# Optimization experiments

Hardware: AMD Instinct MI355X
Metric: run time of the kernel (lower is better)

## Reference

```python
import math
import jax, jax.numpy as jnp
import numpy as np

B, P, L, R = 16, 256, 8, 128  # n_embd = L*R = 1024
H = 4 * L * R                 # MLP hidden = 4096

def new_gelu(x):
    # tanh-approx GELU as in NewGELU
    c = math.sqrt(2.0 / math.pi)
    return 0.5 * x * (1.0 + jnp.tanh(c * (x + 0.044715 * x * x * x)))

def setup_inputs() -> dict:
    key = jax.random.key(0)
    k1, k2, k3 = jax.random.split(key, 3)
    x = jax.random.normal(k1, (B, P, L, R), dtype=jnp.float32)
    W1 = jax.random.normal(k2, (L * R, H), dtype=jnp.float32) * 0.02
    b1 = jnp.zeros((H,), dtype=jnp.float32)
    W2 = jax.random.normal(k3, (H, R), dtype=jnp.float32) * 0.02
    b2 = jnp.zeros((R,), dtype=jnp.float32)
    return {"x": x, "W1": W1, "b1": b1, "W2": W2, "b2": b2}

def reference(x, W1, b1, W2, b2):
    b, p, l, r = x.shape
    flat = x.reshape(b, p, l * r)                       # [B,P,L*R]
    # Level i input = flat with first i*R entries zeroed (zeros-pad + tail slice)
    col = jnp.arange(l * r)
    mask = (col[None, :] >= (jnp.arange(l) * r)[:, None]).astype(x.dtype)  # [L, L*R]
    inp = flat[:, :, None, :] * mask                    # [B,P,L,L*R]
    h = new_gelu(jnp.einsum('bple,eh->bplh', inp, W1) + b1)  # [B,P,L,H]
    out = jnp.einsum('bplh,hr->bplr', h, W2) + b2       # [B,P,L,R]
    return out
```

## Files before the change

### kernel.cpp

```cpp
#include <hip/hip_runtime.h>
#include <hip/hip_bf16.h>


typedef _Float16 half8 __attribute__((ext_vector_type(8)));
typedef _Float16 half4 __attribute__((ext_vector_type(4)));
typedef _Float16 half2v __attribute__((ext_vector_type(2)));
typedef float    f32x4  __attribute__((ext_vector_type(4)));
typedef float    f32x16 __attribute__((ext_vector_type(16)));

#define MFMA3216(A,B,C) __builtin_amdgcn_mfma_f32_32x32x16_f16(A, B, C, 0, 0, 0)
#define MFMA1632(A,B,C) __builtin_amdgcn_mfma_f32_16x16x32_f16(A, B, C, 0, 0, 0)

__device__ __forceinline__ float gelu_f(float x){
  float t2 = x * fmaf(x*x, -0.10294324f, -2.30220842f);
  float e  = __builtin_amdgcn_exp2f(t2);
  return x * __builtin_amdgcn_rcpf(1.0f + e);
}

#define XROW 1028

__global__ void k_prep(const float* __restrict__ x, const float* __restrict__ w1,
                       const float* __restrict__ w2,
                       _Float16* __restrict__ xt, _Float16* __restrict__ w1t,
                       _Float16* __restrict__ w2t){
  __shared__ _Float16 Xs[32*XROW];
  int bid = blockIdx.x;
  int t   = threadIdx.x;
  if (bid < 128){
    const float4* x4 = reinterpret_cast<const float4*>(x) + (size_t)bid*8192;
    #pragma unroll
    for (int i = 0; i < 32; ++i){
      float4 v = x4[i*256 + t];
      half4 h;
      h[0]=(_Float16)v.x; h[1]=(_Float16)v.y; h[2]=(_Float16)v.z; h[3]=(_Float16)v.w;
      *reinterpret_cast<half4*>(Xs + i*XROW + t*4) = h;
    }
    __syncthreads();
    #pragma unroll
    for (int f = 0; f < 16; ++f){
      int fragidx = f*256 + t;
      int lane = fragidx & 63, kf = fragidx >> 6;
      int tok32 = lane & 31;
      int k = kf*16 + (lane >> 5)*8;
      half8 v = *reinterpret_cast<const half8*>(Xs + tok32*XROW + k);
      *reinterpret_cast<half8*>(xt + ((size_t)bid*4096 + fragidx)*8) = v;
    }
  } else if (bid < 2176){
    int tid = (bid - 128)*256 + t;
    int lane = tid & 63;
    int ht   = (tid >> 6) & 15;
    int kf   = (tid >> 10) & 63;
    int hq   = tid >> 16;
    int n = hq*512 + ht*32 + (lane & 31);
    int k = kf*16 + (lane >> 5)*8;
    half8 v;
    #pragma unroll
    for (int jj = 0; jj < 8; ++jj) v[jj] = (_Float16)w1[(size_t)(k + jj)*4096 + n];
    *reinterpret_cast<half8*>(w1t + (size_t)tid*8) = v;
  } else {
    int tid = (bid - 2176)*256 + t;
    int lane = tid & 63;
    int tile = tid >> 6;
    int ntr = tile & 7, kt2 = tile >> 3;
    int n = ntr*16 + (lane & 15);
    int k = kt2*32 + (lane >> 4)*8;
    half8 v;
    #pragma unroll
    for (int jj = 0; jj < 8; ++jj) v[jj] = (_Float16)w2[(size_t)(k + jj)*128 + n];
    *reinterpret_cast<half8*>(w2t + (size_t)tid*8) = v;
  }
}

__global__ void k_init_out(const float* __restrict__ b2, float* __restrict__ out){
  int i = blockIdx.x*256 + threadIdx.x;
  float4 bv = reinterpret_cast<const float4*>(b2)[i & 31];
  reinterpret_cast<float4*>(out)[i] = bv;
}

__global__ void k_reduce(const unsigned* __restrict__ part, const float* __restrict__ b2,
                         float* __restrict__ out){
  int tid = blockIdx.x*256 + threadIdx.x;
  int m16 = tid & 15;
  int rw  = (tid >> 4) & 7;
  int q   = (tid >> 7) & 3;
  int tp  = (tid >> 9) & 1;
  int i   = (tid >> 10) & 3;
  int j   = (tid >> 12) & 7;
  int tt  = tid >> 15;
  float s0 = 0.f, s1 = 0.f;
  #pragma unroll
  for (int hq = 0; hq < 8; ++hq){
    unsigned v = __builtin_nontemporal_load(part + (size_t)hq*2097152 + tid);
    half2v h = __builtin_bit_cast(half2v, v);
    s0 += (float)h[0];
    s1 += (float)h[1];
  }
  int r = rw*16 + m16;
  int tok0 = tt*64 + tp*32 + q*4 + i;
  float bb = b2[r];
  out[(size_t)tok0*1024 + j*128 + r]        = s0 + bb;
  out[(size_t)(tok0 + 16)*1024 + j*128 + r] = s1 + bb;
}

__global__ __launch_bounds__(512, 4) void k_treemlp(
    const _Float16* __restrict__ xt, const _Float16* __restrict__ w1t,
    const _Float16* __restrict__ w2t, const float* __restrict__ b1,
    unsigned* __restrict__ partial, float* __restrict__ out, int use_partial){
  int b    = blockIdx.x;
  int hq   = b & 7;
  int tt   = b >> 3;
  int t    = threadIdx.x;
  int w    = t >> 6;
  int lane = t & 63;
  int t32 = lane & 31, q2 = lane >> 5;
  int m16 = lane & 15, q4 = lane >> 4;

  __shared__ _Float16 Pbuf[32768];

  f32x16 acc1[2][2];
  #pragma unroll
  for (int hf = 0; hf < 2; ++hf){
    int base = hq*512 + (w*2 + hf)*32;
    #pragma unroll
    for (int g = 0; g < 4; ++g){
      float4 bv = *reinterpret_cast<const float4*>(b1 + base + 8*g + 4*q2);
      #pragma unroll
      for (int c = 0; c < 4; ++c){
        acc1[hf][0][g*4 + c] = ((const float*)&bv)[c];
        acc1[hf][1][g*4 + c] = ((const float*)&bv)[c];
      }
    }
  }

  const _Float16* xb0 = xt + ((size_t)(tt*2 + 0)*64)*512 + lane*8;
  const _Float16* xb1 = xt + ((size_t)(tt*2 + 1)*64)*512 + lane*8;
  const _Float16* w1base = w1t + (size_t)hq*65536*8 + (size_t)(w*2)*512 + lane*8;
  const _Float16* w2base = w2t + (size_t)(hq*16*8 + w)*512 + lane*8;

  #pragma unroll
  for (int jr = 0; jr < 8; ++jr){
    int j = 7 - jr;

    #pragma unroll
    for (int s = 0; s < 8; ++s){
      int kf = j*8 + s;
      half8 a0 = *reinterpret_cast<const half8*>(w1base + (size_t)(kf*16    )*512);
      half8 a1 = *reinterpret_cast<const half8*>(w1base + (size_t)(kf*16 + 1)*512);
      half8 x0 = *reinterpret_cast<const half8*>(xb0 + (size_t)kf*512);
      half8 x1 = *reinterpret_cast<const half8*>(xb1 + (size_t)kf*512);
      acc1[0][0] = MFMA3216(a0, x0, acc1[0][0]);
      acc1[0][1] = MFMA3216(a0, x1, acc1[0][1]);
      acc1[1][0] = MFMA3216(a1, x0, acc1[1][0]);
      acc1[1][1] = MFMA3216(a1, x1, acc1[1][1]);
    }

    #pragma unroll
    for (int hf = 0; hf < 2; ++hf){
      int kfp = w*2 + hf;
      #pragma unroll
      for (int tg = 0; tg < 2; ++tg){
        int tf = tg*2 + (t32 >> 4);
        #pragma unroll
        for (int g = 0; g < 4; ++g){
          half4 hv;
          #pragma unroll
          for (int c = 0; c < 4; ++c)
            hv[c] = (_Float16)gelu_f(acc1[hf][tg][g*4 + c]);
          *reinterpret_cast<half4*>(
              Pbuf + ((tf*16 + kfp)*64 + g*16 + (t32 & 15))*8 + 4*q2) = hv;
        }
      }
    }
    __syncthreads();

    f32x4 outJ[4];
    #pragma unroll
    for (int tf = 0; tf < 4; ++tf) outJ[tf] = f32x4{0.f, 0.f, 0.f, 0.f};

    #pragma unroll
    for (int kf = 0; kf < 16; ++kf){
      half8 wf = *reinterpret_cast<const half8*>(w2base + (size_t)kf*4096);
      #pragma unroll
      for (int tf = 0; tf < 4; ++tf){
        half8 a2 = *reinterpret_cast<const half8*>(
            Pbuf + ((tf*16 + kf)*64 + lane)*8);
        outJ[tf] = MFMA1632(a2, wf, outJ[tf]);
      }
    }

    if (use_partial){
      unsigned* pb = partial + (size_t)hq*2097152 + (size_t)tt*32768
                   + (size_t)j*4096 + q4*128 + w*16 + m16;
      #pragma unroll
      for (int i = 0; i < 4; ++i)
        #pragma unroll
        for (int tp = 0; tp < 2; ++tp){
          half2v p;
          p[0] = (_Float16)outJ[tp*2    ][i];
          p[1] = (_Float16)outJ[tp*2 + 1][i];
          __builtin_nontemporal_store(__builtin_bit_cast(unsigned, p),
                                      pb + (size_t)i*1024 + tp*512);
        }
    } else {
      #pragma unroll
      for (int tf = 0; tf < 4; ++tf)
        #pragma unroll
        for (int i = 0; i < 4; ++i){
          int tok = tt*64 + tf*16 + q4*4 + i;
          atomicAdd(out + (size_t)tok*1024 + j*128 + w*16 + m16, outJ[tf][i]);
        }
    }
    __syncthreads();
  }
}

extern "C" void kernel_launch(void* const* d_in, const int* in_sizes, int n_in,
                              void* d_out, int out_size, void* d_ws, size_t ws_size,
                              hipStream_t stream){
  (void)in_sizes; (void)n_in; (void)out_size;
  const float* x  = (const float*)d_in[0];
  const float* W1 = (const float*)d_in[1];
  const float* b1 = (const float*)d_in[2];
  const float* W2 = (const float*)d_in[3];
  const float* b2 = (const float*)d_in[4];
  float* out = (float*)d_out;

  _Float16* xt  = (_Float16*)d_ws;
  _Float16* w1t = xt  + 4194304;
  _Float16* w2t = w1t + 4194304;
  unsigned* partial = (unsigned*)(w2t + 524288);
  const size_t need = (size_t)(4194304 + 4194304 + 524288)*2 + (size_t)16777216*4;
  int use_partial = (ws_size >= need) ? 1 : 0;

  hipLaunchKernelGGL(k_prep, dim3(2432), dim3(256), 0, stream, x, W1, W2, xt, w1t, w2t);
  if (!use_partial)
    hipLaunchKernelGGL(k_init_out, dim3(4096), dim3(256), 0, stream, b2, out);
  hipLaunchKernelGGL(k_treemlp, dim3(512), dim3(512), 0, stream,
                     xt, w1t, w2t, b1, partial, out, use_partial);
  if (use_partial)
    hipLaunchKernelGGL(k_reduce, dim3(8192), dim3(256), 0, stream, partial, b2, out);
}
```

Before: 228.6 us.

## Warp-specialize tree MLP: producer waves for GEMM1+GELU, consumer waves for GEMM2

The block grows to 1024 threads and splits into 8 producer waves and 8 consumer waves. Producers compute the first GEMM with GELU for level L into a double-buffered LDS tile while consumers run the second GEMM for the previous level, so the two stages overlap in a software pipeline. X fragments are staged into double-buffered LDS instead of being read from global memory per wave. The second GEMM switches to 32x32x16 MFMA with a new W2 fragment layout, and the partial-sum/reduce indexing changes to match. LDS use roughly doubles and the larger block may reduce occupancy and raise register pressure.

Result: faster. 216.3 us (-5.3%).

```diff
diff --git a/kernel.cpp b/kernel.cpp
--- a/kernel.cpp
+++ b/kernel.cpp
@@ -9,7 +9,6 @@
 typedef float    f32x16 __attribute__((ext_vector_type(16)));
 
 #define MFMA3216(A,B,C) __builtin_amdgcn_mfma_f32_32x32x16_f16(A, B, C, 0, 0, 0)
-#define MFMA1632(A,B,C) __builtin_amdgcn_mfma_f32_16x16x32_f16(A, B, C, 0, 0, 0)
 
 __device__ __forceinline__ float gelu_f(float x){
   float t2 = x * fmaf(x*x, -0.10294324f, -2.30220842f);
@@ -60,10 +59,11 @@
   } else {
     int tid = (bid - 2176)*256 + t;
     int lane = tid & 63;
-    int tile = tid >> 6;
-    int ntr = tile & 7, kt2 = tile >> 3;
-    int n = ntr*16 + (lane & 15);
-    int k = kt2*32 + (lane >> 4)*8;
+    int rt   = (tid >> 6) & 3;
+    int kf   = (tid >> 8) & 31;
+    int hq   = tid >> 13;
+    int n = rt*32 + (lane & 31);
+    int k = hq*512 + kf*16 + (lane >> 5)*8;
     half8 v;
     #pragma unroll
     for (int jj = 0; jj < 8; ++jj) v[jj] = (_Float16)w2[(size_t)(k + jj)*128 + n];
@@ -80,11 +80,8 @@
 __global__ void k_reduce(const unsigned* __restrict__ part, const float* __restrict__ b2,
                          float* __restrict__ out){
   int tid = blockIdx.x*256 + threadIdx.x;
-  int m16 = tid & 15;
-  int rw  = (tid >> 4) & 7;
-  int q   = (tid >> 7) & 3;
-  int tp  = (tid >> 9) & 1;
-  int i   = (tid >> 10) & 3;
+  int r   = tid & 127;
+  int tc  = (tid >> 7) & 31;
   int j   = (tid >> 12) & 7;
   int tt  = tid >> 15;
   float s0 = 0.f, s1 = 0.f;
@@ -95,14 +92,13 @@
     s0 += (float)h[0];
     s1 += (float)h[1];
   }
-  int r = rw*16 + m16;
-  int tok0 = tt*64 + tp*32 + q*4 + i;
+  int tka = tt*64 + (tc >> 3)*16 + (tc & 7);
   float bb = b2[r];
-  out[(size_t)tok0*1024 + j*128 + r]        = s0 + bb;
-  out[(size_t)(tok0 + 16)*1024 + j*128 + r] = s1 + bb;
-}
-
-__global__ __launch_bounds__(512, 4) void k_treemlp(
+  out[(size_t)tka*1024 + j*128 + r]       = s0 + bb;
+  out[(size_t)(tka+8)*1024 + j*128 + r]   = s1 + bb;
+}
+
+__global__ __launch_bounds__(1024, 4) void k_treemlp(
     const _Float16* __restrict__ xt, const _Float16* __restrict__ w1t,
     const _Float16* __restrict__ w2t, const float* __restrict__ b1,
     unsigned* __restrict__ partial, float* __restrict__ out, int use_partial){
@@ -113,102 +109,120 @@
   int w    = t >> 6;
   int lane = t & 63;
   int t32 = lane & 31, q2 = lane >> 5;
-  int m16 = lane & 15, q4 = lane >> 4;
-
-  __shared__ _Float16 Pbuf[32768];
+
+  __shared__ _Float16 Pbuf[2][32768];
+  __shared__ _Float16 Xls[2][8192];
 
   f32x16 acc1[2][2];
+  if (w < 8){
+    #pragma unroll
+    for (int hf = 0; hf < 2; ++hf){
+      int base = hq*512 + (w*2 + hf)*32;
+      #pragma unroll
+      for (int g = 0; g < 4; ++g){
+        float4 bv = *reinterpret_cast<const float4*>(b1 + base + 8*g + 4*q2);
+        #pragma unroll
+        for (int c = 0; c < 4; ++c){
+          acc1[hf][0][g*4 + c] = ((const float*)&bv)[c];
+          acc1[hf][1][g*4 + c] = ((const float*)&bv)[c];
+        }
+      }
+    }
+  }
+
+  {
+    int lane_s = t & 63, s = (t >> 6) & 7, tgl = (t >> 9) & 1;
+    half8 v = *reinterpret_cast<const half8*>(
+        xt + (size_t)((tt*2 + tgl)*64 + 7*8 + s)*512 + lane_s*8);
+    *reinterpret_cast<half8*>(&Xls[1][(size_t)t*8]) = v;
+  }
+  __syncthreads();
+
+  const _Float16* w1base = w1t + (size_t)hq*524288 + (size_t)(w*2)*512 + lane*8;
+  int wc = w - 8;
+  int th = (wc >> 2) & 1, rt = wc & 3;
+  const _Float16* w2base = w2t + ((size_t)(hq*32)*4 + rt)*512 + lane*8;
+
   #pragma unroll
-  for (int hf = 0; hf < 2; ++hf){
-    int base = hq*512 + (w*2 + hf)*32;
-    #pragma unroll
-    for (int g = 0; g < 4; ++g){
-      float4 bv = *reinterpret_cast<const float4*>(b1 + base + 8*g + 4*q2);
-      #pragma unroll
-      for (int c = 0; c < 4; ++c){
-        acc1[hf][0][g*4 + c] = ((const float*)&bv)[c];
-        acc1[hf][1][g*4 + c] = ((const float*)&bv)[c];
+  for (int k = 0; k < 9; ++k){
+    if (w < 8){
+      if (k <= 7){
+        int L = 7 - k;
+        if (L >= 1){
+          #pragma unroll
+          for (int c = 0; c < 2; ++c){
+            int idx = c*512 + (w*64 + lane);
+            int lane_s = idx & 63, s = (idx >> 6) & 7, tgl = idx >> 9;
+            half8 v = *reinterpret_cast<const half8*>(
+                xt + (size_t)((tt*2 + tgl)*64 + (L-1)*8 + s)*512 + lane_s*8);
+            *reinterpret_cast<half8*>(&Xls[(L-1) & 1][(size_t)idx*8]) = v;
+          }
+        }
+        const _Float16* xb = Xls[L & 1];
+        #pragma unroll
+        for (int s = 0; s < 8; ++s){
+          int kfg = L*8 + s;
+          half8 a0 = *reinterpret_cast<const half8*>(w1base + (size_t)(kfg*16    )*512);
+          half8 a1 = *reinterpret_cast<const half8*>(w1base + (size_t)(kfg*16 + 1)*512);
+          half8 x0 = *reinterpret_cast<const half8*>(&xb[(size_t)((    s)*64 + lane)*8]);
+          half8 x1 = *reinterpret_cast<const half8*>(&xb[(size_t)((8 + s)*64 + lane)*8]);
+          acc1[0][0] = MFMA3216(a0, x0, acc1[0][0]);
+          acc1[0][1] = MFMA3216(a0, x1, acc1[0][1]);
+          acc1[1][0] = MFMA3216(a1, x0, acc1[1][0]);
+          acc1[1][1] = MFMA3216(a1, x1, acc1[1][1]);
+        }
+        _Float16* pb = Pbuf[L & 1];
+        #pragma unroll
+        for (int hf = 0; hf < 2; ++hf)
+          #pragma unroll
+          for (int tg = 0; tg < 2; ++tg)
+            #pragma unroll
+            for (int g2 = 0; g2 < 4; ++g2){
+              half4 hv;
+              #pragma unroll
+              for (int rr = 0; rr < 4; ++rr)
+                hv[rr] = (_Float16)gelu_f(acc1[hf][tg][g2*4 + rr]);
+              int kf = (w*2 + hf)*2 + (g2 >> 1);
+              *reinterpret_cast<half4*>(
+                  &pb[(size_t)((tg*32 + kf)*64 + t32 + 32*(g2 & 1))*8 + 4*q2]) = hv;
+            }
       }
-    }
-  }
-
-  const _Float16* xb0 = xt + ((size_t)(tt*2 + 0)*64)*512 + lane*8;
-  const _Float16* xb1 = xt + ((size_t)(tt*2 + 1)*64)*512 + lane*8;
-  const _Float16* w1base = w1t + (size_t)hq*65536*8 + (size_t)(w*2)*512 + lane*8;
-  const _Float16* w2base = w2t + (size_t)(hq*16*8 + w)*512 + lane*8;
-
-  #pragma unroll
-  for (int jr = 0; jr < 8; ++jr){
-    int j = 7 - jr;
-
-    #pragma unroll
-    for (int s = 0; s < 8; ++s){
-      int kf = j*8 + s;
-      half8 a0 = *reinterpret_cast<const half8*>(w1base + (size_t)(kf*16    )*512);
-      half8 a1 = *reinterpret_cast<const half8*>(w1base + (size_t)(kf*16 + 1)*512);
-      half8 x0 = *reinterpret_cast<const half8*>(xb0 + (size_t)kf*512);
-      half8 x1 = *reinterpret_cast<const half8*>(xb1 + (size_t)kf*512);
-      acc1[0][0] = MFMA3216(a0, x0, acc1[0][0]);
-      acc1[0][1] = MFMA3216(a0, x1, acc1[0][1]);
-      acc1[1][0] = MFMA3216(a1, x0, acc1[1][0]);
-      acc1[1][1] = MFMA3216(a1, x1, acc1[1][1]);
-    }
-
-    #pragma unroll
-    for (int hf = 0; hf < 2; ++hf){
-      int kfp = w*2 + hf;
-      #pragma unroll
-      for (int tg = 0; tg < 2; ++tg){
-        int tf = tg*2 + (t32 >> 4);
-        #pragma unroll
-        for (int g = 0; g < 4; ++g){
-          half4 hv;
-          #pragma unroll
-          for (int c = 0; c < 4; ++c)
-            hv[c] = (_Float16)gelu_f(acc1[hf][tg][g*4 + c]);
-          *reinterpret_cast<half4*>(
-              Pbuf + ((tf*16 + kfp)*64 + g*16 + (t32 & 15))*8 + 4*q2) = hv;
+    } else {
+      if (k >= 1){
+        int Lc = 8 - k;
+        const _Float16* pb = Pbuf[Lc & 1];
+        f32x16 outJ;
+        #pragma unroll
+        for (int c = 0; c < 16; ++c) outJ[c] = 0.f;
+        #pragma unroll
+        for (int kf = 0; kf < 32; ++kf){
+          half8 wf = *reinterpret_cast<const half8*>(w2base + (size_t)kf*2048);
+          half8 pf = *reinterpret_cast<const half8*>(
+              &pb[(size_t)((th*32 + kf)*64 + lane)*8]);
+          outJ = MFMA3216(pf, wf, outJ);
+        }
+        if (use_partial){
+          unsigned* pbase = partial + (size_t)hq*2097152 + (size_t)tt*32768
+                          + (size_t)Lc*4096;
+          #pragma unroll
+          for (int i = 0; i < 8; ++i){
+            int gg = i >> 2, ii = i & 3;
+            int lo = gg*8 + ii;
+            half2v p;
+            p[0] = (_Float16)outJ[lo];
+            p[1] = (_Float16)outJ[lo + 4];
+            int tc = (th*2 + gg)*8 + ii + 4*q2;
+            __builtin_nontemporal_store(__builtin_bit_cast(unsigned, p),
+                                        pbase + (size_t)tc*128 + rt*32 + t32);
+          }
+        } else {
+          #pragma unroll
+          for (int reg = 0; reg < 16; ++reg){
+            int tok = tt*64 + th*32 + (reg & 3) + 8*(reg >> 2) + 4*q2;
+            atomicAdd(out + (size_t)tok*1024 + Lc*128 + rt*32 + t32, outJ[reg]);
+          }
         }
       }
-    }
-    __syncthreads();
-
-    f32x4 outJ[4];
-    #pragma unroll
-    for (int tf = 0; tf < 4; ++tf) outJ[tf] = f32x4{0.f, 0.f, 0.f, 0.f};
-
-    #pragma unroll
-    for (int kf = 0; kf < 16; ++kf){
-      half8 wf = *reinterpret_cast<const half8*>(w2base + (size_t)kf*4096);
-      #pragma unroll
-      for (int tf = 0; tf < 4; ++tf){
-        half8 a2 = *reinterpret_cast<const half8*>(
-            Pbuf + ((tf*16 + kf)*64 + lane)*8);
-        outJ[tf] = MFMA1632(a2, wf, outJ[tf]);
-      }
-    }
-
-    if (use_partial){
-      unsigned* pb = partial + (size_t)hq*2097152 + (size_t)tt*32768
-                   + (size_t)j*4096 + q4*128 + w*16 + m16;
-      #pragma unroll
-      for (int i = 0; i < 4; ++i)
-        #pragma unroll
-        for (int tp = 0; tp < 2; ++tp){
-          half2v p;
-          p[0] = (_Float16)outJ[tp*2    ][i];
-          p[1] = (_Float16)outJ[tp*2 + 1][i];
-          __builtin_nontemporal_store(__builtin_bit_cast(unsigned, p),
-                                      pb + (size_t)i*1024 + tp*512);
-        }
-    } else {
-      #pragma unroll
-      for (int tf = 0; tf < 4; ++tf)
-        #pragma unroll
-        for (int i = 0; i < 4; ++i){
-          int tok = tt*64 + tf*16 + q4*4 + i;
-          atomicAdd(out + (size_t)tok*1024 + j*128 + w*16 + m16, outJ[tf][i]);
-        }
     }
     __syncthreads();
   }
@@ -235,7 +249,7 @@
   hipLaunchKernelGGL(k_prep, dim3(2432), dim3(256), 0, stream, x, W1, W2, xt, w1t, w2t);
   if (!use_partial)
     hipLaunchKernelGGL(k_init_out, dim3(4096), dim3(256), 0, stream, b2, out);
-  hipLaunchKernelGGL(k_treemlp, dim3(512), dim3(512), 0, stream,
+  hipLaunchKernelGGL(k_treemlp, dim3(512), dim3(1024), 0, stream,
                      xt, w1t, w2t, b1, partial, out, use_partial);
   if (use_partial)
     hipLaunchKernelGGL(k_reduce, dim3(8192), dim3(256), 0, stream, partial, b2, out);
```
